# Optimization experiments

Hardware: AMD Instinct MI355X
Metric: run time of the kernel (lower is better)

## Reference

```python
import jax, jax.numpy as jnp
import numpy as np

B, S, D = 16, 2048, 128


def setup_inputs() -> dict:
    k = jax.random.key(0)
    k1, k2, k3, k4 = jax.random.split(k, 4)
    query = jax.random.normal(k1, (B, S, D), dtype=jnp.float32)
    key = jax.random.normal(k2, (B, S, D), dtype=jnp.float32)
    value = jax.random.normal(k3, (B, S, D), dtype=jnp.float32)
    # per-query tensor-valued inverse scale; shift away from zero for stable division
    inv_scale_factor = jax.random.uniform(k4, (B, S, 1), dtype=jnp.float32) + 0.5
    dropout_p = jnp.float32(0.1)
    return {"query": query, "key": key, "value": value,
            "inv_scale_factor": inv_scale_factor, "dropout_p": dropout_p}


def reference(query, key, value, inv_scale_factor, dropout_p):
    # QK^T: [B, Sq, Sk]
    qk = jnp.einsum('bqd,bkd->bqk', query, key)
    # tensor-valued scale divide (broadcast [B, Sq, 1] over keys)
    scaled_qk = qk / inv_scale_factor
    softmax_qk = jax.nn.softmax(scaled_qk, axis=-1)
    # dropout with a fixed RNG key (deterministic reference)
    keep_prob = 1.0 - dropout_p
    mask = jax.random.bernoulli(jax.random.key(42), keep_prob, softmax_qk.shape)
    dropout_qk = jnp.where(mask, softmax_qk / keep_prob, jnp.float32(0.0))
    # AV: [B, Sq, Dv]
    return jnp.einsum('bqk,bkv->bqv', dropout_qk, value)
```

## Files before the change

### kernel.cpp

```cpp
#include <hip/hip_runtime.h>
#include <stdint.h>


#define B_ 16
#define S_ 2048
#define D_ 128
#define TQ 64
#define TK 64
#define KSTR 136
#define VSTR 72
#define PSTR 72

typedef float f32x4 __attribute__((ext_vector_type(4)));
typedef short b16x8 __attribute__((ext_vector_type(8)));

__device__ __forceinline__ uint2 threefry2x32_0_42(uint32_t x0, uint32_t x1) {
  const uint32_t k0 = 0u, k1 = 42u;
  const uint32_t k2 = 0x1BD11BDAu ^ k0 ^ k1;
  x0 += k0; x1 += k1;
#define TFR(r) { x0 += x1; x1 = (x1 << (r)) | (x1 >> (32 - (r))); x1 ^= x0; }
  TFR(13) TFR(15) TFR(26) TFR(6)
  x0 += k1; x1 += k2 + 1u;
  TFR(17) TFR(29) TFR(16) TFR(24)
  x0 += k2; x1 += k0 + 2u;
  TFR(13) TFR(15) TFR(26) TFR(6)
  x0 += k0; x1 += k1 + 3u;
  TFR(17) TFR(29) TFR(16) TFR(24)
  x0 += k1; x1 += k2 + 4u;
  TFR(13) TFR(15) TFR(26) TFR(6)
  x0 += k2; x1 += k0 + 5u;
#undef TFR
  return make_uint2(x0, x1);
}

__device__ __forceinline__ uint32_t jax_bits(uint32_t j) {
  const uint2 tf = threefry2x32_0_42(0u, j);
  return tf.x ^ tf.y;
}

__device__ __forceinline__ uint16_t bf16_rne(float x) {
  const uint32_t u = __float_as_uint(x);
  return (uint16_t)((u + 0x7FFFu + ((u >> 16) & 1u)) >> 16);
}

__global__ __launch_bounds__(256, 2)
void attn_mfma_kernel(const float* __restrict__ Q, const float* __restrict__ K,
                      const float* __restrict__ V, const float* __restrict__ ISF,
                      const float* __restrict__ DP, float* __restrict__ OUT) {
  __shared__ __align__(16) short sKhi[TK * KSTR];
  __shared__ __align__(16) short sKlo[TK * KSTR];
  __shared__ __align__(16) short sVT[D_ * VSTR];
  __shared__ __align__(16) short sP[4 * 16 * PSTR];

  const int t    = threadIdx.x;
  const int w    = t >> 6;
  const int lane = t & 63;
  const int l15  = lane & 15;
  const int quad = lane >> 4;
  const int b    = blockIdx.y;
  const int qw   = blockIdx.x * TQ + w * 16;

  const float kp = 1.0f - DP[0];

  float rsc[4], m_[4], l_[4];
  uint32_t jq[4];
  #pragma unroll
  for (int r = 0; r < 4; ++r) {
    rsc[r] = 1.0f / ISF[b * S_ + qw + quad * 4 + r];
    m_[r] = -INFINITY;
    l_[r] = 0.0f;
    jq[r] = ((uint32_t)b << 22) + (uint32_t)(qw + quad * 4 + r) * (uint32_t)S_;
  }

  b16x8 qhi[4], qlo[4];
  {
    const float* qp = Q + ((size_t)(b * S_ + qw + l15)) * D_;
    #pragma unroll
    for (int c = 0; c < 4; ++c) {
      const float4 a = *(const float4*)(qp + c * 32 + quad * 8);
      const float4 d = *(const float4*)(qp + c * 32 + quad * 8 + 4);
      const float xs[8] = {a.x, a.y, a.z, a.w, d.x, d.y, d.z, d.w};
      #pragma unroll
      for (int j = 0; j < 8; ++j) {
        const uint32_t u = __float_as_uint(xs[j]);
        const float lf = xs[j] - __uint_as_float(u & 0xFFFF0000u);
        qhi[c][j] = (short)(u >> 16);
        qlo[c][j] = (short)(__float_as_uint(lf) >> 16);
      }
    }
  }

  f32x4 accO[8];
  #pragma unroll
  for (int i = 0; i < 8; ++i) accO[i] = (f32x4){0.f, 0.f, 0.f, 0.f};

  short* const pwv = &sP[w * 16 * PSTR];

  for (int kt = 0; kt < S_ / TK; ++kt) {
    __syncthreads();

    {
      const int krow = t >> 2, dseg = (t & 3) * 32;
      const float* gk = K + ((size_t)(b * S_ + kt * TK + krow)) * D_ + dseg;
      #pragma unroll
      for (int u8 = 0; u8 < 4; ++u8) {
        const float4 a = *(const float4*)(gk + u8 * 8);
        const float4 d = *(const float4*)(gk + u8 * 8 + 4);
        const float xs[8] = {a.x, a.y, a.z, a.w, d.x, d.y, d.z, d.w};
        b16x8 hi, lo;
        #pragma unroll
        for (int j = 0; j < 8; ++j) {
          const uint32_t u = __float_as_uint(xs[j]);
          const float lf = xs[j] - __uint_as_float(u & 0xFFFF0000u);
          hi[j] = (short)(u >> 16);
          lo[j] = (short)(__float_as_uint(lf) >> 16);
        }
        *(b16x8*)&sKhi[krow * KSTR + dseg + u8 * 8] = hi;
        *(b16x8*)&sKlo[krow * KSTR + dseg + u8 * 8] = lo;
      }
    }
    {
      const int kp2 = t & 31, dseg = (t >> 5) * 16;
      const float* g0 = V + ((size_t)(b * S_ + kt * TK + 2 * kp2)) * D_ + dseg;
      float v0[16], v1[16];
      #pragma unroll
      for (int u4 = 0; u4 < 4; ++u4) {
        *(float4*)&v0[u4 * 4] = *(const float4*)(g0 + u4 * 4);
        *(float4*)&v1[u4 * 4] = *(const float4*)(g0 + D_ + u4 * 4);
      }
      #pragma unroll
      for (int d = 0; d < 16; ++d) {
        const uint32_t pk = (uint32_t)bf16_rne(v0[d]) |
                            ((uint32_t)bf16_rne(v1[d]) << 16);
        *(uint32_t*)&sVT[(dseg + d) * VSTR + 2 * kp2] = pk;
      }
    }
    __syncthreads();

    f32x4 s[4];
    #pragma unroll
    for (int n = 0; n < 4; ++n) {
      f32x4 acc = (f32x4){0.f, 0.f, 0.f, 0.f};
      #pragma unroll
      for (int c = 0; c < 4; ++c) {
        const b16x8 bh = *(const b16x8*)&sKhi[(n * 16 + l15) * KSTR + c * 32 + quad * 8];
        const b16x8 bl = *(const b16x8*)&sKlo[(n * 16 + l15) * KSTR + c * 32 + quad * 8];
        acc = __builtin_amdgcn_mfma_f32_16x16x32_bf16(qhi[c], bh, acc, 0, 0, 0);
        acc = __builtin_amdgcn_mfma_f32_16x16x32_bf16(qhi[c], bl, acc, 0, 0, 0);
        acc = __builtin_amdgcn_mfma_f32_16x16x32_bf16(qlo[c], bh, acc, 0, 0, 0);
      }
      s[n] = acc;
    }

    float mx[4];
    #pragma unroll
    for (int r = 0; r < 4; ++r) {
      s[0][r] *= rsc[r]; s[1][r] *= rsc[r]; s[2][r] *= rsc[r]; s[3][r] *= rsc[r];
      mx[r] = fmaxf(fmaxf(s[0][r], s[1][r]), fmaxf(s[2][r], s[3][r]));
    }
    #pragma unroll
    for (int off = 1; off < 16; off <<= 1) {
      #pragma unroll
      for (int r = 0; r < 4; ++r) mx[r] = fmaxf(mx[r], __shfl_xor(mx[r], off, 16));
    }
    float alpha[4], rs[4];
    #pragma unroll
    for (int r = 0; r < 4; ++r) {
      const float mnew = fmaxf(m_[r], mx[r]);
      alpha[r] = __expf(m_[r] - mnew);
      m_[r] = mnew;
      rs[r] = 0.f;
    }
    #pragma unroll
    for (int n = 0; n < 4; ++n) {
      #pragma unroll
      for (int r = 0; r < 4; ++r) {
        const float p = __expf(s[n][r] - m_[r]);
        s[n][r] = p;
        rs[r] += p;
      }
    }
    #pragma unroll
    for (int off = 1; off < 16; off <<= 1) {
      #pragma unroll
      for (int r = 0; r < 4; ++r) rs[r] += __shfl_xor(rs[r], off, 16);
    }
    #pragma unroll
    for (int r = 0; r < 4; ++r) l_[r] = l_[r] * alpha[r] + rs[r];
    #pragma unroll
    for (int i = 0; i < 8; ++i) {
      #pragma unroll
      for (int r = 0; r < 4; ++r) accO[i][r] *= alpha[r];
    }

    #pragma unroll
    for (int n = 0; n < 4; ++n) {
      const int col = n * 16 + l15;
      #pragma unroll
      for (int r = 0; r < 4; ++r) {
        const uint32_t bits = jax_bits(jq[r] + (uint32_t)(kt * TK + col));
        const float uni = __uint_as_float((bits >> 9) | 0x3F800000u) - 1.0f;
        const uint16_t pb = bf16_rne(s[n][r]);
        pwv[(quad * 4 + r) * PSTR + col] = (uni < kp) ? (short)pb : (short)0;
      }
    }
    __threadfence_block();

    #pragma unroll
    for (int ks = 0; ks < 2; ++ks) {
      const b16x8 ap = *(const b16x8*)&pwv[l15 * PSTR + ks * 32 + quad * 8];
      #pragma unroll
      for (int d8 = 0; d8 < 8; ++d8) {
        const b16x8 bv = *(const b16x8*)&sVT[(d8 * 16 + l15) * VSTR + ks * 32 + quad * 8];
        accO[d8] = __builtin_amdgcn_mfma_f32_16x16x32_bf16(ap, bv, accO[d8], 0, 0, 0);
      }
    }
  }

  float inv[4];
  #pragma unroll
  for (int r = 0; r < 4; ++r) inv[r] = 1.0f / (l_[r] * kp);
  float* op = OUT + ((size_t)(b * S_ + qw)) * D_;
  #pragma unroll
  for (int d8 = 0; d8 < 8; ++d8) {
    #pragma unroll
    for (int r = 0; r < 4; ++r)
      op[(quad * 4 + r) * D_ + d8 * 16 + l15] = accO[d8][r] * inv[r];
  }
}

extern "C" void kernel_launch(void* const* d_in, const int* in_sizes, int n_in,
                              void* d_out, int out_size, void* d_ws, size_t ws_size,
                              hipStream_t stream) {
  const float* q   = (const float*)d_in[0];
  const float* k   = (const float*)d_in[1];
  const float* v   = (const float*)d_in[2];
  const float* isf = (const float*)d_in[3];
  const float* dp  = (const float*)d_in[4];
  float* out = (float*)d_out;

  dim3 grid(S_ / TQ, B_);
  attn_mfma_kernel<<<grid, dim3(256), 0, stream>>>(q, k, v, isf, dp, out);
}
```

Before: 345.2 us.

## Prefetch next K/V tile into registers, fold scale into Q, use packed bf16 conversion

Global loads for the next K/V tile are now issued into registers right after the LDS barrier, so their latency overlaps the current tile's MFMA and softmax work. The per-row inverse scale is folded into Q before the hi/lo bf16 split, which removes the per-tile score multiply. Manual bf16 rounding is replaced with packed hardware conversions, and the dropout test becomes an integer compare against a precomputed threshold. The register prefetch buffers add about 64 VGPRs per thread, which can pressure occupancy under launch_bounds(256,2). Folding the scale into Q also changes rounding slightly.

```diff
diff --git a/kernel.cpp b/kernel.cpp
--- a/kernel.cpp
+++ b/kernel.cpp
@@ -1,4 +1,5 @@
 #include <hip/hip_runtime.h>
+#include <hip/hip_bf16.h>
 #include <stdint.h>
 
 
@@ -13,6 +14,16 @@
 
 typedef float f32x4 __attribute__((ext_vector_type(4)));
 typedef short b16x8 __attribute__((ext_vector_type(8)));
+
+union U4B8 { uint32_t u[4]; b16x8 v; };
+union F32R { float4 q[8]; float f[32]; };
+union F16R { float4 q[4]; float f[16]; };
+
+__device__ __forceinline__ uint32_t pk_bf16(float a, float b) {
+  union { __hip_bfloat162 h; uint32_t u; } c;
+  c.h = __float22bfloat162_rn(make_float2(a, b));
+  return c.u;
+}
 
 __device__ __forceinline__ uint2 threefry2x32_0_42(uint32_t x0, uint32_t x1) {
   const uint32_t k0 = 0u, k1 = 42u;
@@ -38,11 +49,6 @@
   return tf.x ^ tf.y;
 }
 
-__device__ __forceinline__ uint16_t bf16_rne(float x) {
-  const uint32_t u = __float_as_uint(x);
-  return (uint16_t)((u + 0x7FFFu + ((u >> 16) & 1u)) >> 16);
-}
-
 __global__ __launch_bounds__(256, 2)
 void attn_mfma_kernel(const float* __restrict__ Q, const float* __restrict__ K,
                       const float* __restrict__ V, const float* __restrict__ ISF,
@@ -61,12 +67,12 @@
   const int qw   = blockIdx.x * TQ + w * 16;
 
   const float kp = 1.0f - DP[0];
-
-  float rsc[4], m_[4], l_[4];
+  const uint32_t TH = __float_as_uint(1.0f + kp) & 0x7FFFFFu;
+
+  float m_[4], l_[4];
   uint32_t jq[4];
   #pragma unroll
   for (int r = 0; r < 4; ++r) {
-    rsc[r] = 1.0f / ISF[b * S_ + qw + quad * 4 + r];
     m_[r] = -INFINITY;
     l_[r] = 0.0f;
     jq[r] = ((uint32_t)b << 22) + (uint32_t)(qw + quad * 4 + r) * (uint32_t)S_;
@@ -74,19 +80,25 @@
 
   b16x8 qhi[4], qlo[4];
   {
+    const float qs = 1.0f / ISF[b * S_ + qw + l15];
     const float* qp = Q + ((size_t)(b * S_ + qw + l15)) * D_;
     #pragma unroll
     for (int c = 0; c < 4; ++c) {
       const float4 a = *(const float4*)(qp + c * 32 + quad * 8);
       const float4 d = *(const float4*)(qp + c * 32 + quad * 8 + 4);
-      const float xs[8] = {a.x, a.y, a.z, a.w, d.x, d.y, d.z, d.w};
-      #pragma unroll
-      for (int j = 0; j < 8; ++j) {
-        const uint32_t u = __float_as_uint(xs[j]);
-        const float lf = xs[j] - __uint_as_float(u & 0xFFFF0000u);
-        qhi[c][j] = (short)(u >> 16);
-        qlo[c][j] = (short)(__float_as_uint(lf) >> 16);
-      }
+      float xs[8] = {a.x, a.y, a.z, a.w, d.x, d.y, d.z, d.w};
+      U4B8 hi, lo;
+      #pragma unroll
+      for (int p = 0; p < 4; ++p) {
+        const float x0 = xs[2 * p] * qs, x1 = xs[2 * p + 1] * qs;
+        const uint32_t h = pk_bf16(x0, x1);
+        const float r0 = x0 - __uint_as_float(h << 16);
+        const float r1 = x1 - __uint_as_float(h & 0xFFFF0000u);
+        hi.u[p] = h;
+        lo.u[p] = pk_bf16(r0, r1);
+      }
+      qhi[c] = hi.v;
+      qlo[c] = lo.v;
     }
   }
 
@@ -95,47 +107,58 @@
   for (int i = 0; i < 8; ++i) accO[i] = (f32x4){0.f, 0.f, 0.f, 0.f};
 
   short* const pwv = &sP[w * 16 * PSTR];
+
+  const int krow = t >> 2, kcol = (t & 3) * 32;
+  const int vkey = 2 * (t & 31), vseg = (t >> 5) * 16;
+
+  F32R kreg;
+  F16R vreg0, vreg1;
+
+#define ISSUE_LOADS(KT)                                                        \
+  {                                                                            \
+    const float4* gk4 = (const float4*)(K +                                    \
+        ((size_t)(b * S_ + (KT) * TK + krow)) * D_ + kcol);                    \
+    _Pragma("unroll") for (int i = 0; i < 8; ++i) kreg.q[i] = gk4[i];          \
+    const float4* gv4 = (const float4*)(V +                                    \
+        ((size_t)(b * S_ + (KT) * TK + vkey)) * D_ + vseg);                    \
+    _Pragma("unroll") for (int i = 0; i < 4; ++i) {                            \
+      vreg0.q[i] = gv4[i];                                                     \
+      vreg1.q[i] = gv4[i + 32];                \
+    }                                                                          \
+  }
+
+  ISSUE_LOADS(0)
 
   for (int kt = 0; kt < S_ / TK; ++kt) {
     __syncthreads();
 
     {
-      const int krow = t >> 2, dseg = (t & 3) * 32;
-      const float* gk = K + ((size_t)(b * S_ + kt * TK + krow)) * D_ + dseg;
-      #pragma unroll
-      for (int u8 = 0; u8 < 4; ++u8) {
-        const float4 a = *(const float4*)(gk + u8 * 8);
-        const float4 d = *(const float4*)(gk + u8 * 8 + 4);
-        const float xs[8] = {a.x, a.y, a.z, a.w, d.x, d.y, d.z, d.w};
-        b16x8 hi, lo;
+      short* kh = &sKhi[krow * KSTR + kcol];
+      short* kl = &sKlo[krow * KSTR + kcol];
+      #pragma unroll
+      for (int g = 0; g < 4; ++g) {
+        U4B8 hi, lo;
         #pragma unroll
-        for (int j = 0; j < 8; ++j) {
-          const uint32_t u = __float_as_uint(xs[j]);
-          const float lf = xs[j] - __uint_as_float(u & 0xFFFF0000u);
-          hi[j] = (short)(u >> 16);
-          lo[j] = (short)(__float_as_uint(lf) >> 16);
+        for (int p = 0; p < 4; ++p) {
+          const float x0 = kreg.f[g * 8 + 2 * p], x1 = kreg.f[g * 8 + 2 * p + 1];
+          const uint32_t h = pk_bf16(x0, x1);
+          const float r0 = x0 - __uint_as_float(h << 16);
+          const float r1 = x1 - __uint_as_float(h & 0xFFFF0000u);
+          hi.u[p] = h;
+          lo.u[p] = pk_bf16(r0, r1);
         }
-        *(b16x8*)&sKhi[krow * KSTR + dseg + u8 * 8] = hi;
-        *(b16x8*)&sKlo[krow * KSTR + dseg + u8 * 8] = lo;
+        *(b16x8*)&kh[g * 8] = hi.v;
+        *(b16x8*)&kl[g * 8] = lo.v;
       }
     }
     {
-      const int kp2 = t & 31, dseg = (t >> 5) * 16;
-      const float* g0 = V + ((size_t)(b * S_ + kt * TK + 2 * kp2)) * D_ + dseg;
-      float v0[16], v1[16];
-      #pragma unroll
-      for (int u4 = 0; u4 < 4; ++u4) {
-        *(float4*)&v0[u4 * 4] = *(const float4*)(g0 + u4 * 4);
-        *(float4*)&v1[u4 * 4] = *(const float4*)(g0 + D_ + u4 * 4);
-      }
-      #pragma unroll
-      for (int d = 0; d < 16; ++d) {
-        const uint32_t pk = (uint32_t)bf16_rne(v0[d]) |
-                            ((uint32_t)bf16_rne(v1[d]) << 16);
-        *(uint32_t*)&sVT[(dseg + d) * VSTR + 2 * kp2] = pk;
-      }
+      #pragma unroll
+      for (int d = 0; d < 16; ++d)
+        *(uint32_t*)&sVT[(vseg + d) * VSTR + vkey] = pk_bf16(vreg0.f[d], vreg1.f[d]);
     }
     __syncthreads();
+
+    if (kt + 1 < S_ / TK) ISSUE_LOADS(kt + 1)
 
     f32x4 s[4];
     #pragma unroll
@@ -154,10 +177,8 @@
 
     float mx[4];
     #pragma unroll
-    for (int r = 0; r < 4; ++r) {
-      s[0][r] *= rsc[r]; s[1][r] *= rsc[r]; s[2][r] *= rsc[r]; s[3][r] *= rsc[r];
+    for (int r = 0; r < 4; ++r)
       mx[r] = fmaxf(fmaxf(s[0][r], s[1][r]), fmaxf(s[2][r], s[3][r]));
-    }
     #pragma unroll
     for (int off = 1; off < 16; off <<= 1) {
       #pragma unroll
@@ -196,13 +217,19 @@
     #pragma unroll
     for (int n = 0; n < 4; ++n) {
       const int col = n * 16 + l15;
+      const uint32_t jcol = (uint32_t)(kt * TK + col);
+      float pf[4];
       #pragma unroll
       for (int r = 0; r < 4; ++r) {
-        const uint32_t bits = jax_bits(jq[r] + (uint32_t)(kt * TK + col));
-        const float uni = __uint_as_float((bits >> 9) | 0x3F800000u) - 1.0f;
-        const uint16_t pb = bf16_rne(s[n][r]);
-        pwv[(quad * 4 + r) * PSTR + col] = (uni < kp) ? (short)pb : (short)0;
-      }
+        const uint32_t bits = jax_bits(jq[r] + jcol);
+        pf[r] = ((bits >> 9) < TH) ? s[n][r] : 0.0f;
+      }
+      const uint32_t pk01 = pk_bf16(pf[0], pf[1]);
+      const uint32_t pk23 = pk_bf16(pf[2], pf[3]);
+      pwv[(quad * 4 + 0) * PSTR + col] = (short)(uint16_t)pk01;
+      pwv[(quad * 4 + 1) * PSTR + col] = (short)(uint16_t)(pk01 >> 16);
+      pwv[(quad * 4 + 2) * PSTR + col] = (short)(uint16_t)pk23;
+      pwv[(quad * 4 + 3) * PSTR + col] = (short)(uint16_t)(pk23 >> 16);
     }
     __threadfence_block();
 
@@ -216,6 +243,7 @@
       }
     }
   }
+#undef ISSUE_LOADS
 
   float inv[4];
   #pragma unroll
```

Result: no change. 342.4 us (-0.8%).
